# Kernel optimization log

Measured on AMD Instinct MI355X. Metric: run time of the kernel, lower is better.

Reference implementation:

```python
import jax, jax.numpy as jnp
import numpy as np

N_NODES = 100000
N_EDGES = 1600000
MUL = 32            # channel multiplicity for every irrep
INV_SQRT_MUL = 1.0 / np.sqrt(32.0)
# path constants: wigner-3j norms (1/sqrt3 for 0x1->1 and 1x1->0, 1/sqrt6 for 1x1->1)
# combined with fan-in path normalization (fan=32 for 0e out, fan=64 for 1o out, 2 paths)
C_DOT = 1.0 / np.sqrt(3.0 * 32.0)
C_SCL = 1.0 / np.sqrt(3.0 * 64.0)
C_CRS = 1.0 / np.sqrt(6.0 * 64.0)


def setup_inputs() -> dict:
    key = jax.random.key(0)
    ks = jax.random.split(key, 12)
    x = jax.random.normal(ks[0], (N_NODES, 128), jnp.float32)
    pos = jax.random.normal(ks[1], (N_NODES, 3), jnp.float32)
    edge_index = jax.random.randint(ks[2], (2, N_EDGES), 0, N_NODES, jnp.int32)
    # o3.Linear(32x0e+32x1o -> 32x0e+32x0e+32x1o): per-irrep channel mixing
    W_node_s = jax.random.normal(ks[3], (32, 64), jnp.float32)   # 0e -> (scalars|gates)
    W_node_v = jax.random.normal(ks[4], (32, 32), jnp.float32)   # 1o -> 1o
    # FullyConnectedTensorProduct(32x0e+32x1o, 1x1o -> 32x0e+32x1o): 3 CG paths
    W_tp_d = jax.random.normal(ks[5], (32, 32), jnp.float32)     # 1o x 1o -> 0e (dot)
    W_tp_s = jax.random.normal(ks[6], (32, 32), jnp.float32)     # 0e x 1o -> 1o
    W_tp_c = jax.random.normal(ks[7], (32, 32), jnp.float32)     # 1o x 1o -> 1o (cross)
    # o3.Linear(32x0e+32x1o -> 32x0e+32x1o)
    W_msg_s = jax.random.normal(ks[8], (32, 32), jnp.float32)
    W_msg_v = jax.random.normal(ks[9], (32, 32), jnp.float32)
    ln_gamma = jnp.ones((128,), jnp.float32)
    ln_beta = jnp.zeros((128,), jnp.float32)
    return {"x": x, "pos": pos, "edge_index": edge_index,
            "W_node_s": W_node_s, "W_node_v": W_node_v,
            "W_tp_d": W_tp_d, "W_tp_s": W_tp_s, "W_tp_c": W_tp_c,
            "W_msg_s": W_msg_s, "W_msg_v": W_msg_v,
            "ln_gamma": ln_gamma, "ln_beta": ln_beta}


def reference(x, pos, edge_index, W_node_s, W_node_v, W_tp_d, W_tp_s, W_tp_c,
              W_msg_s, W_msg_v, ln_gamma, ln_beta):
    N = x.shape[0]
    row, col = edge_index[0], edge_index[1]
    # split node irreps: 32 scalars (0e) | 32 vectors (1o) of dim 3
    s = x[:, :32]                       # [N,32]
    v = x[:, 32:].reshape(-1, 32, 3)    # [N,32,3]
    # lin_node (equivariant linear, path-normalized by 1/sqrt(fan_in)=1/sqrt(32))
    h_s = (s @ W_node_s) * INV_SQRT_MUL                          # [N,64]
    h_v = jnp.einsum('nid,ij->njd', v, W_node_v) * INV_SQRT_MUL  # [N,32,3]
    # Gate: relu scalars, sigmoid gates multiply the gated vectors
    sc = jax.nn.relu(h_s[:, :32])                                # [N,32]
    hv = h_v * jax.nn.sigmoid(h_s[:, 32:])[:, :, None]           # [N,32,3]
    # spherical harmonics l=1, component norm: sqrt(3)*unit vec in e3nn (y,z,x) order
    rel = pos[col] - pos[row]                                    # [E,3]
    unit = rel / jnp.sqrt(jnp.sum(rel * rel, -1, keepdims=True) + 1e-12)
    u = jnp.sqrt(3.0) * unit[:, (1, 2, 0)]                       # [E,3]
    # gather source-node features per edge
    sj = sc[col]                                                 # [E,32]
    vj = hv[col]                                                 # [E,32,3]
    # CG tensor product paths
    dot = jnp.einsum('eid,ed->ei', vj, u)                        # 1o x 1o -> 0e
    crs = jnp.cross(vj, u[:, None, :])                           # 1o x 1o -> 1o
    m0 = (dot @ W_tp_d) * C_DOT                                  # [E,32]
    m1 = (sj @ W_tp_s)[:, :, None] * u[:, None, :] * C_SCL \
         + jnp.einsum('eid,ik->ekd', crs, W_tp_c) * C_CRS        # [E,32,3]
    m = jnp.concatenate([m0, m1.reshape(-1, 96)], -1)            # [E,128]
    # scatter-mean over destination nodes (row)
    deg = jax.ops.segment_sum(jnp.ones_like(row, jnp.float32), row,
                              num_segments=N).clip(1.0)
    mi = jax.ops.segment_sum(m, row, num_segments=N) / deg[:, None]
    # lin_msg
    ms = (mi[:, :32] @ W_msg_s) * INV_SQRT_MUL
    mv = jnp.einsum('nid,ij->njd', mi[:, 32:].reshape(-1, 32, 3),
                    W_msg_v) * INV_SQRT_MUL
    o = jnp.concatenate([ms, mv.reshape(-1, 96)], -1)            # [N,128]
    # LayerNorm over 128 dims (as in the original, affine)
    mu = o.mean(-1, keepdims=True)
    var = o.var(-1, keepdims=True)
    o = (o - mu) / jnp.sqrt(var + 1e-5) * ln_gamma + ln_beta
    return x + o
```

## Files before the change

kernel.cpp:

```cpp
#include <hip/hip_runtime.h>
#include <math.h>


static constexpr float INV_SQRT_MUL = 0.17677669529663687f;
static constexpr float C_DOT = 0.10206207261596575f;
static constexpr float C_SCL = 0.07216878364870322f;
static constexpr float C_CRS = 0.05103103630798288f;
static constexpr float SQRT3 = 1.7320508075688772f;
static constexpr int MAXDEG = 48;
static constexpr int SCAT_B = 2048;
static constexpr int CNT_WORDS = 8 * 16384;

#define WS_ALIGN(x) (((x) + 255) & ~(size_t)255)
#define CIDX(r) ((((r) & 7) << 14) | ((r) >> 3))

__device__ __forceinline__ unsigned short f2bf(float v) {
    unsigned int b = __float_as_uint(v);
    b += 0x7FFFu + ((b >> 16) & 1u);
    return (unsigned short)(b >> 16);
}
__device__ __forceinline__ float bf2f(unsigned short u) {
    return __uint_as_float(((unsigned int)u) << 16);
}

__global__ __launch_bounds__(1024)
void fuse_w(const float* __restrict__ Wns, const float* __restrict__ Wnv,
            const float* __restrict__ Wtpd, const float* __restrict__ Wtps,
            const float* __restrict__ Wtpc, const float* __restrict__ Wms,
            const float* __restrict__ Wmv, float* __restrict__ Wall) {
    int t = threadIdx.x;
    int i = t >> 5, j = t & 31;
    float a = 0.f, b = 0.f, c = 0.f;
#pragma unroll
    for (int k = 0; k < 32; ++k) {
        a += Wtpd[i * 32 + k] * Wms[k * 32 + j];
        b += Wtps[i * 32 + k] * Wmv[k * 32 + j];
        c += Wtpc[i * 32 + k] * Wmv[k * 32 + j];
    }
    Wall[t]        = a * (C_DOT * INV_SQRT_MUL);
    Wall[1024 + t] = b * (C_SCL * INV_SQRT_MUL);
    Wall[2048 + t] = c * (C_CRS * INV_SQRT_MUL);
    int i2 = t >> 5, k2 = t & 31;
    Wall[3072 + t]        = Wns[k2 * 64 + i2];
    Wall[3072 + 1024 + t] = Wns[k2 * 64 + 32 + i2];
    Wall[5120 + t]        = Wnv[k2 * 32 + i2];
}

__global__ __launch_bounds__(256)
void scatter(const int* __restrict__ eidx, int* __restrict__ cnt,
             int* __restrict__ slots, int E) {
    int shard = blockIdx.x & 7;
    int tid = (blockIdx.x >> 3) * 256 + threadIdx.x;
    const int SSTRIDE = (SCAT_B / 8) * 256;
    int Q = E >> 2;
    const int4* r4p = (const int4*)eidx;
    const int4* c4p = (const int4*)(eidx + E);
    for (int q = tid; q < Q; q += SSTRIDE) {
        int4 R = r4p[q];
        bool any = ((R.x & 7) == shard) | ((R.y & 7) == shard) |
                   ((R.z & 7) == shard) | ((R.w & 7) == shard);
        if (!any) continue;
        int4 C = c4p[q];
        int rr[4] = {R.x, R.y, R.z, R.w};
        int cc[4] = {C.x, C.y, C.z, C.w};
#pragma unroll
        for (int k = 0; k < 4; ++k) {
            if ((rr[k] & 7) == shard) {
                int p = atomicAdd(&cnt[CIDX(rr[k])], 1);
                if (p < MAXDEG) slots[(size_t)rr[k] * MAXDEG + p] = cc[k];
            }
        }
    }
    for (int e = (Q << 2) + tid; e < E; e += SSTRIDE) {
        int r = eidx[e];
        if ((r & 7) == shard) {
            int c = eidx[E + e];
            int p = atomicAdd(&cnt[CIDX(r)], 1);
            if (p < MAXDEG) slots[(size_t)r * MAXDEG + p] = c;
        }
    }
}

__global__ __launch_bounds__(256)
void node_feat(const float* __restrict__ x, const float* __restrict__ WT,
               ushort4* __restrict__ feat4, int N) {
    __shared__ float buf[4][64 * 36];
    int t = threadIdx.x;
    int wv = t >> 6, l = t & 63;
    float* bw = buf[wv];
    int nt = (N + 63) >> 6;
    int tile = blockIdx.x * 4 + wv;
    if (tile >= nt) return;
    int B = tile << 6;
    int r0 = l >> 3, cw = (l & 7) << 2;
    const float* WnsT = WT;
    const float* WnvT = WT + 2048;

    auto stage = [&](int w0) {
#pragma unroll
        for (int j = 0; j < 8; ++j) {
            int row = j * 8 + r0;
            int node = B + row;
            float4 v = make_float4(0.f, 0.f, 0.f, 0.f);
            if (node < N) v = *(const float4*)(x + (size_t)node * 128 + w0 + cw);
            *(float4*)(bw + row * 36 + cw) = v;
        }
        __builtin_amdgcn_wave_barrier();
    };
    auto readrow = [&](float* dst) {
        const float4* rp = (const float4*)(bw + l * 36);
#pragma unroll
        for (int j = 0; j < 8; ++j) {
            float4 q = rp[j];
            dst[4*j] = q.x; dst[4*j+1] = q.y; dst[4*j+2] = q.z; dst[4*j+3] = q.w;
        }
        __builtin_amdgcn_wave_barrier();
    };

    float xs[32];
    stage(0); readrow(xs);
    unsigned int scp[16];
    float sig[32];
#pragma unroll 2
    for (int i = 0; i < 32; ++i) {
        float a = 0.f, g = 0.f;
#pragma unroll
        for (int k = 0; k < 32; ++k) {
            a += xs[k] * WnsT[i * 32 + k];
            g += xs[k] * WnsT[(32 + i) * 32 + k];
        }
        a = fmaxf(a * INV_SQRT_MUL, 0.f);
        float s = 1.f / (1.f + __expf(-g * INV_SQRT_MUL));
        unsigned short s16 = f2bf(a);
        if ((i & 1) == 0) scp[i >> 1] = s16;
        else scp[i >> 1] |= ((unsigned int)s16) << 16;
        sig[i] = s * INV_SQRT_MUL;
    }
    float xv[96];
    stage(32); readrow(xv);
    stage(64); readrow(xv + 32);
    stage(96); readrow(xv + 64);
    int node = B + l;
    bool liv = (node < N);
#pragma unroll 2
    for (int i = 0; i < 32; ++i) {
        float o0 = 0.f, o1 = 0.f, o2 = 0.f;
#pragma unroll
        for (int k = 0; k < 32; ++k) {
            float w = WnvT[i * 32 + k];
            o0 += xv[3 * k + 0] * w;
            o1 += xv[3 * k + 1] * w;
            o2 += xv[3 * k + 2] * w;
        }
        float s = sig[i];
        unsigned int scw = scp[i >> 1];
        ushort4 pk;
        pk.x = (unsigned short)((i & 1) ? (scw >> 16) : (scw & 0xFFFFu));
        pk.y = f2bf(o0 * s); pk.z = f2bf(o1 * s); pk.w = f2bf(o2 * s);
        if (liv) feat4[(size_t)node * 32 + i] = pk;
    }
}

__global__ __launch_bounds__(256)
void agg(const float* __restrict__ x, const float* __restrict__ pos,
         const ushort4* __restrict__ feat4, const int* __restrict__ cnt,
         const int* __restrict__ slots, const float* __restrict__ Wall,
         const float* __restrict__ gamma, const float* __restrict__ beta,
         float* __restrict__ out, int N) {
    __shared__ float4 cu[4][MAXDEG];
    __shared__ float4 finA[4][32];
    __shared__ float4 finB[4][32];
    int t = threadIdx.x;
    int wv = t >> 6, lane = t & 63;
    int ch = lane & 31, slot = lane >> 5;
    int n = blockIdx.x * 4 + wv;
    bool live = (n < N);
    int nn = live ? n : 0;
    int deg = cnt[CIDX(nn)];
    if (!live) deg = 0;
    int c = min(deg, MAXDEG);

    float prx = pos[nn * 3 + 0], pry = pos[nn * 3 + 1], prz = pos[nn * 3 + 2];
    if (lane < c) {
        int col = slots[(size_t)nn * MAXDEG + lane];
        float rx = pos[col * 3 + 0] - prx, ry = pos[col * 3 + 1] - pry, rz = pos[col * 3 + 2] - prz;
        float inv = rsqrtf(rx * rx + ry * ry + rz * rz + 1e-12f) * SQRT3;
        cu[wv][lane] = make_float4(ry * inv, rz * inv, rx * inv, __int_as_float(col << 8));
    }
    __builtin_amdgcn_wave_barrier();

    const char* featB = (const char*)feat4;
    unsigned int ch8 = (unsigned int)ch * 8u;
    const float4* cuw = cu[wv];
    float D = 0.f, S0 = 0.f, S1 = 0.f, S2 = 0.f, C0 = 0.f, C1 = 0.f, C2 = 0.f;

    auto body = [&](const float4& q, const ushort4& f) {
        float u0 = q.x, u1 = q.y, u2 = q.z;
        float sj = bf2f(f.x);
        float h0 = bf2f(f.y), h1 = bf2f(f.z), h2 = bf2f(f.w);
        D  += h0 * u0 + h1 * u1 + h2 * u2;
        S0 += sj * u0; S1 += sj * u1; S2 += sj * u2;
        C0 += h1 * u2 - h2 * u1;
        C1 += h2 * u0 - h0 * u2;
        C2 += h0 * u1 - h1 * u0;
    };

    int jb = 0;
    for (; jb + 8 <= c; jb += 8) {
        float4 q[4]; ushort4 f[4];
#pragma unroll
        for (int k = 0; k < 4; ++k) q[k] = cuw[jb + 2 * k + slot];
#pragma unroll
        for (int k = 0; k < 4; ++k)
            f[k] = *(const ushort4*)(featB + (__float_as_uint(q[k].w) + ch8));
#pragma unroll
        for (int k = 0; k < 4; ++k) body(q[k], f[k]);
    }
    for (int j = jb + slot; j < c; j += 2) {
        float4 q = cuw[j];
        ushort4 f = *(const ushort4*)(featB + (__float_as_uint(q.w) + ch8));
        body(q, f);
    }

    D  += __shfl_xor(D, 32);
    S0 += __shfl_xor(S0, 32); S1 += __shfl_xor(S1, 32); S2 += __shfl_xor(S2, 32);
    C0 += __shfl_xor(C0, 32); C1 += __shfl_xor(C1, 32); C2 += __shfl_xor(C2, 32);
    if (lane < 32) {
        finA[wv][ch] = make_float4(D, S0, S1, S2);
        finB[wv][ch] = make_float4(C0, C1, C2, 0.f);
    }
    __builtin_amdgcn_wave_barrier();

    float invdeg = 1.0f / (float)((deg > 0) ? deg : 1);
    float a0 = 0.f, aV0 = 0.f, aV1 = 0.f, aV2 = 0.f;
    int i0 = slot << 4;
#pragma unroll 8
    for (int ii = 0; ii < 16; ++ii) {
        int i = i0 + ii;
        float4 a = finA[wv][i];
        float4 b = finB[wv][i];
        float wd = Wall[i * 32 + ch];
        float ws = Wall[1024 + i * 32 + ch];
        float wc = Wall[2048 + i * 32 + ch];
        a0  += a.x * wd;
        aV0 += a.y * ws + b.x * wc;
        aV1 += a.z * ws + b.y * wc;
        aV2 += a.w * ws + b.z * wc;
    }
    a0  += __shfl_xor(a0, 32);
    aV0 += __shfl_xor(aV0, 32); aV1 += __shfl_xor(aV1, 32); aV2 += __shfl_xor(aV2, 32);

    float vd = a0 * invdeg;
    float v0 = aV0 * invdeg, v1 = aV1 * invdeg, v2 = aV2 * invdeg;

    float s1 = vd + v0 + v1 + v2;
    float s2 = vd * vd + v0 * v0 + v1 * v1 + v2 * v2;
#pragma unroll
    for (int m = 16; m >= 1; m >>= 1) {
        s1 += __shfl_xor(s1, m);
        s2 += __shfl_xor(s2, m);
    }
    float mu = s1 * (1.f / 128.f);
    float var = s2 * (1.f / 128.f) - mu * mu;
    float rstd = rsqrtf(var + 1e-5f);

    if (live && lane < 32) {
        size_t base = (size_t)n * 128;
        int chv = 32 + ch * 3;
        float xv0 = __builtin_nontemporal_load(&x[base + ch]);
        float xa  = __builtin_nontemporal_load(&x[base + chv + 0]);
        float xb  = __builtin_nontemporal_load(&x[base + chv + 1]);
        float xc  = __builtin_nontemporal_load(&x[base + chv + 2]);
        __builtin_nontemporal_store(xv0 + (vd - mu) * rstd * gamma[ch] + beta[ch], &out[base + ch]);
        __builtin_nontemporal_store(xa + (v0 - mu) * rstd * gamma[chv + 0] + beta[chv + 0], &out[base + chv + 0]);
        __builtin_nontemporal_store(xb + (v1 - mu) * rstd * gamma[chv + 1] + beta[chv + 1], &out[base + chv + 1]);
        __builtin_nontemporal_store(xc + (v2 - mu) * rstd * gamma[chv + 2] + beta[chv + 2], &out[base + chv + 2]);
    }
}

extern "C" void kernel_launch(void* const* d_in, const int* in_sizes, int n_in,
                              void* d_out, int out_size, void* d_ws, size_t ws_size,
                              hipStream_t stream) {
    const float* x     = (const float*)d_in[0];
    const float* pos   = (const float*)d_in[1];
    const int*   eidx  = (const int*)d_in[2];
    const float* Wns   = (const float*)d_in[3];
    const float* Wnv   = (const float*)d_in[4];
    const float* Wtpd  = (const float*)d_in[5];
    const float* Wtps  = (const float*)d_in[6];
    const float* Wtpc  = (const float*)d_in[7];
    const float* Wms   = (const float*)d_in[8];
    const float* Wmv   = (const float*)d_in[9];
    const float* gamma = (const float*)d_in[10];
    const float* beta  = (const float*)d_in[11];
    float* out = (float*)d_out;

    int N = in_sizes[0] / 128;
    int E = in_sizes[2] / 2;

    char* ws = (char*)d_ws;
    size_t off = 0;
    unsigned short* feat = (unsigned short*)(ws + off); off += WS_ALIGN((size_t)N * 128 * 2);
    int*   cnt  = (int*)(ws + off);   off += WS_ALIGN((size_t)CNT_WORDS * 4);
    float* Wall = (float*)(ws + off); off += WS_ALIGN(6144 * 4);
    int*   slots = (int*)(ws + off);

    hipMemsetAsync(cnt, 0, (size_t)CNT_WORDS * 4, stream);
    fuse_w<<<1, 1024, 0, stream>>>(Wns, Wnv, Wtpd, Wtps, Wtpc, Wms, Wmv, Wall);
    scatter<<<SCAT_B, 256, 0, stream>>>(eidx, cnt, slots, E);
    int nt = (N + 63) >> 6;
    node_feat<<<(nt + 3) / 4, 256, 0, stream>>>(x, Wall + 3072, (ushort4*)feat, N);
    agg<<<(N + 3) / 4, 256, 0, stream>>>(x, pos, (const ushort4*)feat, cnt, slots, Wall, gamma, beta, out, N);
}
```

Before: 411.2 us.

## Merge scatter and node-feature kernels into one launch; pad agg edge loop

The edge-scatter and node-feature kernels become a single launch in which half the blocks do the scatter and half loop persistently over node tiles, so the atomic-bound scatter and the compute-bound feature pass can run concurrently. In agg, the slot load is hoisted and issued alongside the count and position loads, and the edge loop is padded to a multiple of 8 with zeroed dummy entries, which removes the remainder loop. That padding needs the slots buffer cleared, so an extra memset of N*48*4 bytes is added. Each half now gets only 1024 blocks, launch bounds on agg add an occupancy hint, and padded edges do wasted gathers of node 0.

```diff
diff --git a/kernel.cpp b/kernel.cpp
--- a/kernel.cpp
+++ b/kernel.cpp
@@ -8,7 +8,7 @@
 static constexpr float C_CRS = 0.05103103630798288f;
 static constexpr float SQRT3 = 1.7320508075688772f;
 static constexpr int MAXDEG = 48;
-static constexpr int SCAT_B = 2048;
+static constexpr int COMB_B = 2048;
 static constexpr int CNT_WORDS = 8 * 16384;
 
 #define WS_ALIGN(x) (((x) + 255) & ~(size_t)255)
@@ -47,121 +47,124 @@
 }
 
 __global__ __launch_bounds__(256)
-void scatter(const int* __restrict__ eidx, int* __restrict__ cnt,
-             int* __restrict__ slots, int E) {
-    int shard = blockIdx.x & 7;
-    int tid = (blockIdx.x >> 3) * 256 + threadIdx.x;
-    const int SSTRIDE = (SCAT_B / 8) * 256;
-    int Q = E >> 2;
-    const int4* r4p = (const int4*)eidx;
-    const int4* c4p = (const int4*)(eidx + E);
-    for (int q = tid; q < Q; q += SSTRIDE) {
-        int4 R = r4p[q];
-        bool any = ((R.x & 7) == shard) | ((R.y & 7) == shard) |
-                   ((R.z & 7) == shard) | ((R.w & 7) == shard);
-        if (!any) continue;
-        int4 C = c4p[q];
-        int rr[4] = {R.x, R.y, R.z, R.w};
-        int cc[4] = {C.x, C.y, C.z, C.w};
-#pragma unroll
-        for (int k = 0; k < 4; ++k) {
-            if ((rr[k] & 7) == shard) {
-                int p = atomicAdd(&cnt[CIDX(rr[k])], 1);
-                if (p < MAXDEG) slots[(size_t)rr[k] * MAXDEG + p] = cc[k];
+void phase1(const float* __restrict__ x, const float* __restrict__ WT,
+            const int* __restrict__ eidx, ushort4* __restrict__ feat4,
+            int* __restrict__ cnt, int* __restrict__ slots, int N, int E) {
+    __shared__ float buf[4][64 * 36];
+    int t = threadIdx.x;
+
+    if ((blockIdx.x & 8) == 0) {
+        int shard = blockIdx.x & 7;
+        int sid = (int)(blockIdx.x >> 4);
+        int tid = sid * 256 + t;
+        const int SSTRIDE = (COMB_B / 16) * 256;
+        int Q = E >> 2;
+        const int4* r4p = (const int4*)eidx;
+        const int4* c4p = (const int4*)(eidx + E);
+        for (int q = tid; q < Q; q += SSTRIDE) {
+            int4 R = r4p[q];
+            bool any = ((R.x & 7) == shard) | ((R.y & 7) == shard) |
+                       ((R.z & 7) == shard) | ((R.w & 7) == shard);
+            if (!any) continue;
+            int4 C = c4p[q];
+            int rr[4] = {R.x, R.y, R.z, R.w};
+            int cc[4] = {C.x, C.y, C.z, C.w};
+#pragma unroll
+            for (int k = 0; k < 4; ++k) {
+                if ((rr[k] & 7) == shard) {
+                    int p = atomicAdd(&cnt[CIDX(rr[k])], 1);
+                    if (p < MAXDEG) slots[(size_t)rr[k] * MAXDEG + p] = cc[k];
+                }
             }
         }
-    }
-    for (int e = (Q << 2) + tid; e < E; e += SSTRIDE) {
-        int r = eidx[e];
-        if ((r & 7) == shard) {
-            int c = eidx[E + e];
-            int p = atomicAdd(&cnt[CIDX(r)], 1);
-            if (p < MAXDEG) slots[(size_t)r * MAXDEG + p] = c;
+        for (int e = (Q << 2) + tid; e < E; e += SSTRIDE) {
+            int r = eidx[e];
+            if ((r & 7) == shard) {
+                int c = eidx[E + e];
+                int p = atomicAdd(&cnt[CIDX(r)], 1);
+                if (p < MAXDEG) slots[(size_t)r * MAXDEG + p] = c;
+            }
         }
-    }
-}
-
-__global__ __launch_bounds__(256)
-void node_feat(const float* __restrict__ x, const float* __restrict__ WT,
-               ushort4* __restrict__ feat4, int N) {
-    __shared__ float buf[4][64 * 36];
-    int t = threadIdx.x;
-    int wv = t >> 6, l = t & 63;
-    float* bw = buf[wv];
-    int nt = (N + 63) >> 6;
-    int tile = blockIdx.x * 4 + wv;
-    if (tile >= nt) return;
-    int B = tile << 6;
-    int r0 = l >> 3, cw = (l & 7) << 2;
-    const float* WnsT = WT;
-    const float* WnvT = WT + 2048;
-
-    auto stage = [&](int w0) {
-#pragma unroll
-        for (int j = 0; j < 8; ++j) {
-            int row = j * 8 + r0;
-            int node = B + row;
-            float4 v = make_float4(0.f, 0.f, 0.f, 0.f);
-            if (node < N) v = *(const float4*)(x + (size_t)node * 128 + w0 + cw);
-            *(float4*)(bw + row * 36 + cw) = v;
+    } else {
+        int fid = (int)(((blockIdx.x >> 4) << 3) | (blockIdx.x & 7));
+        int wv = t >> 6, l = t & 63;
+        float* bw = buf[wv];
+        int nt = (N + 63) >> 6;
+        int r0 = l >> 3, cw = (l & 7) << 2;
+        const float* WnsT = WT;
+        const float* WnvT = WT + 2048;
+
+        for (int tile = fid * 4 + wv; tile < nt; tile += (COMB_B / 2) * 4) {
+            int B = tile << 6;
+            auto stage = [&](int w0) {
+#pragma unroll
+                for (int j = 0; j < 8; ++j) {
+                    int row = j * 8 + r0;
+                    int node = B + row;
+                    float4 v = make_float4(0.f, 0.f, 0.f, 0.f);
+                    if (node < N) v = *(const float4*)(x + (size_t)node * 128 + w0 + cw);
+                    *(float4*)(bw + row * 36 + cw) = v;
+                }
+                __builtin_amdgcn_wave_barrier();
+            };
+            auto readrow = [&](float* dst) {
+                const float4* rp = (const float4*)(bw + l * 36);
+#pragma unroll
+                for (int j = 0; j < 8; ++j) {
+                    float4 q = rp[j];
+                    dst[4*j] = q.x; dst[4*j+1] = q.y; dst[4*j+2] = q.z; dst[4*j+3] = q.w;
+                }
+                __builtin_amdgcn_wave_barrier();
+            };
+
+            float xs[32];
+            stage(0); readrow(xs);
+            unsigned int scp[16];
+            float sig[32];
+#pragma unroll 2
+            for (int i = 0; i < 32; ++i) {
+                float a = 0.f, g = 0.f;
+#pragma unroll
+                for (int k = 0; k < 32; ++k) {
+                    a += xs[k] * WnsT[i * 32 + k];
+                    g += xs[k] * WnsT[(32 + i) * 32 + k];
+                }
+                a = fmaxf(a * INV_SQRT_MUL, 0.f);
+                float s = 1.f / (1.f + __expf(-g * INV_SQRT_MUL));
+                unsigned short s16 = f2bf(a);
+                if ((i & 1) == 0) scp[i >> 1] = s16;
+                else scp[i >> 1] |= ((unsigned int)s16) << 16;
+                sig[i] = s * INV_SQRT_MUL;
+            }
+            float xv[96];
+            stage(32); readrow(xv);
+            stage(64); readrow(xv + 32);
+            stage(96); readrow(xv + 64);
+            int node = B + l;
+            bool liv = (node < N);
+#pragma unroll 2
+            for (int i = 0; i < 32; ++i) {
+                float o0 = 0.f, o1 = 0.f, o2 = 0.f;
+#pragma unroll
+                for (int k = 0; k < 32; ++k) {
+                    float w = WnvT[i * 32 + k];
+                    o0 += xv[3 * k + 0] * w;
+                    o1 += xv[3 * k + 1] * w;
+                    o2 += xv[3 * k + 2] * w;
+                }
+                float s = sig[i];
+                unsigned int scw = scp[i >> 1];
+                ushort4 pk;
+                pk.x = (unsigned short)((i & 1) ? (scw >> 16) : (scw & 0xFFFFu));
+                pk.y = f2bf(o0 * s); pk.z = f2bf(o1 * s); pk.w = f2bf(o2 * s);
+                if (liv) feat4[(size_t)node * 32 + i] = pk;
+            }
+            __builtin_amdgcn_wave_barrier();
         }
-        __builtin_amdgcn_wave_barrier();
-    };
-    auto readrow = [&](float* dst) {
-        const float4* rp = (const float4*)(bw + l * 36);
-#pragma unroll
-        for (int j = 0; j < 8; ++j) {
-            float4 q = rp[j];
-            dst[4*j] = q.x; dst[4*j+1] = q.y; dst[4*j+2] = q.z; dst[4*j+3] = q.w;
-        }
-        __builtin_amdgcn_wave_barrier();
-    };
-
-    float xs[32];
-    stage(0); readrow(xs);
-    unsigned int scp[16];
-    float sig[32];
-#pragma unroll 2
-    for (int i = 0; i < 32; ++i) {
-        float a = 0.f, g = 0.f;
-#pragma unroll
-        for (int k = 0; k < 32; ++k) {
-            a += xs[k] * WnsT[i * 32 + k];
-            g += xs[k] * WnsT[(32 + i) * 32 + k];
-        }
-        a = fmaxf(a * INV_SQRT_MUL, 0.f);
-        float s = 1.f / (1.f + __expf(-g * INV_SQRT_MUL));
-        unsigned short s16 = f2bf(a);
-        if ((i & 1) == 0) scp[i >> 1] = s16;
-        else scp[i >> 1] |= ((unsigned int)s16) << 16;
-        sig[i] = s * INV_SQRT_MUL;
-    }
-    float xv[96];
-    stage(32); readrow(xv);
-    stage(64); readrow(xv + 32);
-    stage(96); readrow(xv + 64);
-    int node = B + l;
-    bool liv = (node < N);
-#pragma unroll 2
-    for (int i = 0; i < 32; ++i) {
-        float o0 = 0.f, o1 = 0.f, o2 = 0.f;
-#pragma unroll
-        for (int k = 0; k < 32; ++k) {
-            float w = WnvT[i * 32 + k];
-            o0 += xv[3 * k + 0] * w;
-            o1 += xv[3 * k + 1] * w;
-            o2 += xv[3 * k + 2] * w;
-        }
-        float s = sig[i];
-        unsigned int scw = scp[i >> 1];
-        ushort4 pk;
-        pk.x = (unsigned short)((i & 1) ? (scw >> 16) : (scw & 0xFFFFu));
-        pk.y = f2bf(o0 * s); pk.z = f2bf(o1 * s); pk.w = f2bf(o2 * s);
-        if (liv) feat4[(size_t)node * 32 + i] = pk;
-    }
-}
-
-__global__ __launch_bounds__(256)
+    }
+}
+
+__global__ __launch_bounds__(256, 8)
 void agg(const float* __restrict__ x, const float* __restrict__ pos,
          const ushort4* __restrict__ feat4, const int* __restrict__ cnt,
          const int* __restrict__ slots, const float* __restrict__ Wall,
@@ -176,16 +179,20 @@
     int n = blockIdx.x * 4 + wv;
     bool live = (n < N);
     int nn = live ? n : 0;
+
     int deg = cnt[CIDX(nn)];
+    int colr = (lane < MAXDEG) ? slots[(size_t)nn * MAXDEG + lane] : 0;
+    float prx = pos[nn * 3 + 0], pry = pos[nn * 3 + 1], prz = pos[nn * 3 + 2];
     if (!live) deg = 0;
     int c = min(deg, MAXDEG);
-
-    float prx = pos[nn * 3 + 0], pry = pos[nn * 3 + 1], prz = pos[nn * 3 + 2];
+    int cpad = (c + 7) & ~7;
+
     if (lane < c) {
-        int col = slots[(size_t)nn * MAXDEG + lane];
-        float rx = pos[col * 3 + 0] - prx, ry = pos[col * 3 + 1] - pry, rz = pos[col * 3 + 2] - prz;
+        float rx = pos[colr * 3 + 0] - prx, ry = pos[colr * 3 + 1] - pry, rz = pos[colr * 3 + 2] - prz;
         float inv = rsqrtf(rx * rx + ry * ry + rz * rz + 1e-12f) * SQRT3;
-        cu[wv][lane] = make_float4(ry * inv, rz * inv, rx * inv, __int_as_float(col << 8));
+        cu[wv][lane] = make_float4(ry * inv, rz * inv, rx * inv, __int_as_float(colr << 8));
+    } else if (lane < MAXDEG) {
+        cu[wv][lane] = make_float4(0.f, 0.f, 0.f, __int_as_float(0));
     }
     __builtin_amdgcn_wave_barrier();
 
@@ -194,19 +201,7 @@
     const float4* cuw = cu[wv];
     float D = 0.f, S0 = 0.f, S1 = 0.f, S2 = 0.f, C0 = 0.f, C1 = 0.f, C2 = 0.f;
 
-    auto body = [&](const float4& q, const ushort4& f) {
-        float u0 = q.x, u1 = q.y, u2 = q.z;
-        float sj = bf2f(f.x);
-        float h0 = bf2f(f.y), h1 = bf2f(f.z), h2 = bf2f(f.w);
-        D  += h0 * u0 + h1 * u1 + h2 * u2;
-        S0 += sj * u0; S1 += sj * u1; S2 += sj * u2;
-        C0 += h1 * u2 - h2 * u1;
-        C1 += h2 * u0 - h0 * u2;
-        C2 += h0 * u1 - h1 * u0;
-    };
-
-    int jb = 0;
-    for (; jb + 8 <= c; jb += 8) {
+    for (int jb = 0; jb < cpad; jb += 8) {
         float4 q[4]; ushort4 f[4];
 #pragma unroll
         for (int k = 0; k < 4; ++k) q[k] = cuw[jb + 2 * k + slot];
@@ -214,12 +209,16 @@
         for (int k = 0; k < 4; ++k)
             f[k] = *(const ushort4*)(featB + (__float_as_uint(q[k].w) + ch8));
 #pragma unroll
-        for (int k = 0; k < 4; ++k) body(q[k], f[k]);
-    }
-    for (int j = jb + slot; j < c; j += 2) {
-        float4 q = cuw[j];
-        ushort4 f = *(const ushort4*)(featB + (__float_as_uint(q.w) + ch8));
-        body(q, f);
+        for (int k = 0; k < 4; ++k) {
+            float u0 = q[k].x, u1 = q[k].y, u2 = q[k].z;
+            float sj = bf2f(f[k].x);
+            float h0 = bf2f(f[k].y), h1 = bf2f(f[k].z), h2 = bf2f(f[k].w);
+            D  += h0 * u0 + h1 * u1 + h2 * u2;
+            S0 += sj * u0; S1 += sj * u1; S2 += sj * u2;
+            C0 += h1 * u2 - h2 * u1;
+            C1 += h2 * u0 - h0 * u2;
+            C2 += h0 * u1 - h1 * u0;
+        }
     }
 
     D  += __shfl_xor(D, 32);
@@ -304,11 +303,11 @@
     int*   cnt  = (int*)(ws + off);   off += WS_ALIGN((size_t)CNT_WORDS * 4);
     float* Wall = (float*)(ws + off); off += WS_ALIGN(6144 * 4);
     int*   slots = (int*)(ws + off);
+    size_t slots_bytes = (size_t)N * MAXDEG * 4 + 256;
 
     hipMemsetAsync(cnt, 0, (size_t)CNT_WORDS * 4, stream);
+    hipMemsetAsync(slots, 0, slots_bytes, stream);
     fuse_w<<<1, 1024, 0, stream>>>(Wns, Wnv, Wtpd, Wtps, Wtpc, Wms, Wmv, Wall);
-    scatter<<<SCAT_B, 256, 0, stream>>>(eidx, cnt, slots, E);
-    int nt = (N + 63) >> 6;
-    node_feat<<<(nt + 3) / 4, 256, 0, stream>>>(x, Wall + 3072, (ushort4*)feat, N);
+    phase1<<<COMB_B, 256, 0, stream>>>(x, Wall + 3072, eidx, (ushort4*)feat, cnt, slots, N, E);
     agg<<<(N + 3) / 4, 256, 0, stream>>>(x, pos, (const ushort4*)feat, cnt, slots, Wall, gamma, beta, out, N);
 }
```

Result: slower. 447.4 us (+8.8%).
